# Kernel optimization log

Measured on AMD Instinct MI355X. Metric: run time of the kernel, lower is better.

## Reference

```python
import jax, jax.numpy as jnp
import numpy as np

BN_EPS = 1e-5


def setup_inputs() -> dict:
    key = jax.random.key(0)
    ks = jax.random.split(key, 8)
    B, S, D = 2048, 64, 128      # batch, seq_len, d_in
    H, DK = 8, 16                # n_head, d_k; H*DK == 128
    F = H * DK
    std = np.sqrt(2.0 / DK).astype(np.float32)
    return {
        "v": jax.random.normal(ks[0], (B, S, D), jnp.float32),
        "Wq": jax.random.normal(ks[1], (F, D), jnp.float32) * std,
        "bq": jnp.zeros((F,), jnp.float32),
        "bn_gamma": jnp.ones((F,), jnp.float32),
        "bn_beta": jnp.zeros((F,), jnp.float32),
        "W2": jax.random.normal(ks[2], (F, F), jnp.float32) * (1.0 / np.sqrt(F)),
        "b2": jnp.zeros((F,), jnp.float32),
        "Wk": jax.random.normal(ks[3], (F, D), jnp.float32) * std,
        "bk": jnp.zeros((F,), jnp.float32),
    }


def reference(v, Wq, bq, bn_gamma, bn_beta, W2, b2, Wk, bk):
    # v: [B, S, D]
    B, S, D = v.shape
    F = Wq.shape[0]
    H = 8
    DK = F // H
    temperature = jnp.asarray(np.sqrt(DK), v.dtype)

    # q path: linear -> mean over seq -> BatchNorm1d (batch stats) -> linear
    q = jnp.einsum("bsd,fd->bsf", v, Wq) + bq          # [B, S, F]
    q = q.mean(axis=1)                                  # [B, F]
    mu = q.mean(axis=0)
    var = q.var(axis=0)                                 # biased, as BN uses
    q = (q - mu) * jax.lax.rsqrt(var + BN_EPS) * bn_gamma + bn_beta
    q = jnp.einsum("bf,gf->bg", q, W2) + b2             # [B, F]
    q = q.reshape(B, H, DK).transpose(1, 0, 2)          # [H, B, DK]

    # k path
    k = (jnp.einsum("bsd,fd->bsf", v, Wk) + bk).reshape(B, S, H, DK)
    k = k.transpose(2, 0, 1, 3)                         # [H, B, S, DK]

    # single query per (head, batch): scores over seq
    attn = jnp.einsum("hbd,hbsd->hbs", q, k) / temperature
    attn = jax.nn.softmax(attn, axis=-1)                # [H, B, S]
    # dropout is identity in eval mode

    # weighted sum over seq of the ORIGINAL v (torch repeats v per head;
    # broadcasting avoids materializing the repeat)
    out = jnp.einsum("hbs,bsd->hbd", attn, v)           # [H, B, D]
    return out, attn
```

## Files before the change

kernel.cpp:

```cpp
#include <hip/hip_runtime.h>

#define B_ 2048
#define S_ 64
#define D_ 128
#define F_ 128
#define H_ 8

__global__ __launch_bounds__(256) void k_q1(const float* __restrict__ v,
                                            const float* __restrict__ Wq,
                                            const float* __restrict__ bq,
                                            float* __restrict__ q1) {
  const int b = blockIdx.x;
  const int t = threadIdx.x;
  __shared__ float red[8 * 128];
  __shared__ __align__(16) float vbarL[128];

  const int c4 = t & 31;
  const int r0 = t >> 5;
  const float4* v4 = (const float4*)(v + (size_t)b * (S_ * D_));
  float4 acc = {0.f, 0.f, 0.f, 0.f};
  #pragma unroll
  for (int i = 0; i < 8; ++i) {
    float4 x = v4[(r0 * 8 + i) * 32 + c4];
    acc.x += x.x; acc.y += x.y; acc.z += x.z; acc.w += x.w;
  }
  red[r0 * 128 + c4 * 4 + 0] = acc.x;
  red[r0 * 128 + c4 * 4 + 1] = acc.y;
  red[r0 * 128 + c4 * 4 + 2] = acc.z;
  red[r0 * 128 + c4 * 4 + 3] = acc.w;
  __syncthreads();
  if (t < 128) {
    float s = 0.f;
    #pragma unroll
    for (int r = 0; r < 8; ++r) s += red[r * 128 + t];
    vbarL[t] = s * (1.0f / 64.0f);
  }
  __syncthreads();

  const float4* Wq4 = (const float4*)Wq;
  const float4* vb4 = (const float4*)vbarL;
  const int d4 = t & 31;
  const int fg = t >> 5;
  #pragma unroll
  for (int fi = 0; fi < 16; ++fi) {
    int f = fi * 8 + fg;
    float4 w = Wq4[f * 32 + d4];
    float4 vv = vb4[d4];
    float p = w.x * vv.x + w.y * vv.y + w.z * vv.z + w.w * vv.w;
    #pragma unroll
    for (int off = 16; off; off >>= 1) p += __shfl_down(p, off, 32);
    if (d4 == 0) q1[b * F_ + f] = p + bq[f];
  }
}

__global__ __launch_bounds__(256) void k_stats(const float* __restrict__ q1,
                                               const float* __restrict__ gamma,
                                               const float* __restrict__ beta,
                                               float* __restrict__ sscale,
                                               float* __restrict__ sshift) {
  const int f = blockIdx.x;
  const int t = threadIdx.x;
  float s = 0.f, sq = 0.f;
  #pragma unroll
  for (int i = 0; i < 8; ++i) {
    float x = q1[(i * 256 + t) * F_ + f];
    s += x;
    sq += x * x;
  }
  #pragma unroll
  for (int off = 32; off; off >>= 1) {
    s += __shfl_down(s, off, 64);
    sq += __shfl_down(sq, off, 64);
  }
  __shared__ float rs_[4], rq_[4];
  const int w = t >> 6;
  if ((t & 63) == 0) { rs_[w] = s; rq_[w] = sq; }
  __syncthreads();
  if (t == 0) {
    s = rs_[0] + rs_[1] + rs_[2] + rs_[3];
    sq = rq_[0] + rq_[1] + rq_[2] + rq_[3];
    float mu = s * (1.0f / (float)B_);
    float var = sq * (1.0f / (float)B_) - mu * mu;
    float rsg = rsqrtf(var + 1e-5f) * gamma[f];
    sscale[f] = rsg;
    sshift[f] = beta[f] - mu * rsg;
  }
}

__global__ __launch_bounds__(256) void k_qw(const float* __restrict__ q1,
                                            const float* __restrict__ sscale,
                                            const float* __restrict__ sshift,
                                            const float* __restrict__ W2,
                                            const float* __restrict__ b2,
                                            const float* __restrict__ Wk,
                                            const float* __restrict__ bk,
                                            float* __restrict__ qW,
                                            float* __restrict__ qb) {
  const int b0 = blockIdx.x * 8;
  const int t = threadIdx.x;
  __shared__ __align__(16) float W2L[128 * 128];
  __shared__ __align__(16) float qnL[8 * 128];
  __shared__ __align__(16) float q2L[8 * 128];

  float4* W2L4 = (float4*)W2L;
  const float4* W2g4 = (const float4*)W2;
  #pragma unroll
  for (int i = 0; i < 16; ++i) {
    int idx4 = i * 256 + t;
    int g = idx4 >> 5, f4 = idx4 & 31;
    W2L4[g * 32 + (f4 ^ (g & 31))] = W2g4[idx4];
  }
  #pragma unroll
  for (int i = 0; i < 4; ++i) {
    int idx = i * 256 + t;
    int bi = idx >> 7, f = idx & 127;
    qnL[idx] = q1[(b0 + bi) * F_ + f] * sscale[f] + sshift[f];
  }
  __syncthreads();

  const float4* qnL4 = (const float4*)qnL;
  #pragma unroll
  for (int i = 0; i < 4; ++i) {
    int o = i * 256 + t;
    int bi = o >> 7, g = o & 127;
    float acc = b2[g];
    #pragma unroll
    for (int f4 = 0; f4 < 32; ++f4) {
      float4 qv = qnL4[bi * 32 + f4];
      float4 wv = W2L4[g * 32 + (f4 ^ (g & 31))];
      acc += qv.x * wv.x + qv.y * wv.y + qv.z * wv.z + qv.w * wv.w;
    }
    q2L[bi * 128 + g] = acc;
  }
  __syncthreads();

  const float4* Wk4 = (const float4*)Wk;
  #pragma unroll
  for (int i = 0; i < 8; ++i) {
    int o4 = i * 256 + t;
    int bi = o4 >> 8, h = (o4 >> 5) & 7, d4 = o4 & 31;
    float4 acc = {0.f, 0.f, 0.f, 0.f};
    const float* q2row = &q2L[bi * 128 + h * 16];
    #pragma unroll
    for (int dk = 0; dk < 16; ++dk) {
      float q = q2row[dk];
      float4 w = Wk4[(h * 16 + dk) * 32 + d4];
      acc.x += q * w.x; acc.y += q * w.y; acc.z += q * w.z; acc.w += q * w.w;
    }
    ((float4*)qW)[(size_t)(b0 + bi) * 256 + h * 32 + d4] = acc;
  }
  if (t < 64) {
    int bi = t >> 3, h = t & 7;
    float acc = 0.f;
    #pragma unroll
    for (int dk = 0; dk < 16; ++dk)
      acc += q2L[bi * 128 + h * 16 + dk] * bk[h * 16 + dk];
    qb[(b0 + bi) * 8 + h] = acc;
  }
}

__global__ __launch_bounds__(256) void k_attn(const float* __restrict__ v,
                                              const float* __restrict__ qW,
                                              const float* __restrict__ qb,
                                              float* __restrict__ outp) {
  const int b = blockIdx.x;
  const int t = threadIdx.x;
  __shared__ __align__(16) float vL[64 * 128];
  __shared__ __align__(16) float qWL[8 * 128];
  __shared__ float attnL[8 * 64];
  __shared__ float qbL[8];

  float4* vL4 = (float4*)vL;
  const float4* vg4 = (const float4*)(v + (size_t)b * (S_ * D_));
  #pragma unroll
  for (int i = 0; i < 8; ++i) {
    int idx = i * 256 + t;
    int s = idx >> 5, c4 = idx & 31;
    vL4[s * 32 + (c4 ^ (s & 31))] = vg4[idx];
  }
  {
    const float4* qWg4 = (const float4*)(qW + (size_t)b * (H_ * D_));
    ((float4*)qWL)[t] = qWg4[t];
  }
  if (t < 8) qbL[t] = qb[b * 8 + t];
  __syncthreads();

  const int s = t & 63;
  const int hq = t >> 6;
  const int h0 = hq * 2, h1 = hq * 2 + 1;
  const float4* qWL4 = (const float4*)qWL;
  float a0 = 0.f, a1 = 0.f;
  #pragma unroll
  for (int d4 = 0; d4 < 32; ++d4) {
    float4 vv = vL4[s * 32 + (d4 ^ (s & 31))];
    float4 w0 = qWL4[h0 * 32 + d4];
    float4 w1 = qWL4[h1 * 32 + d4];
    a0 += vv.x * w0.x + vv.y * w0.y + vv.z * w0.z + vv.w * w0.w;
    a1 += vv.x * w1.x + vv.y * w1.y + vv.z * w1.z + vv.w * w1.w;
  }
  float l0 = (a0 + qbL[h0]) * 0.25f;
  float l1 = (a1 + qbL[h1]) * 0.25f;

  float m0 = l0, m1 = l1;
  #pragma unroll
  for (int off = 32; off; off >>= 1) {
    m0 = fmaxf(m0, __shfl_xor(m0, off, 64));
    m1 = fmaxf(m1, __shfl_xor(m1, off, 64));
  }
  float e0 = __expf(l0 - m0), e1 = __expf(l1 - m1);
  float s0 = e0, s1 = e1;
  #pragma unroll
  for (int off = 32; off; off >>= 1) {
    s0 += __shfl_xor(s0, off, 64);
    s1 += __shfl_xor(s1, off, 64);
  }
  float at0 = e0 / s0, at1 = e1 / s1;
  attnL[h0 * 64 + s] = at0;
  attnL[h1 * 64 + s] = at1;
  float* attn_out = outp + (size_t)H_ * B_ * D_;
  attn_out[(size_t)h0 * (B_ * S_) + b * S_ + s] = at0;
  attn_out[(size_t)h1 * (B_ * S_) + b * S_ + s] = at1;
  __syncthreads();

  const int d4o = t & 31;
  const int h = t >> 5;
  float4 acc = {0.f, 0.f, 0.f, 0.f};
  #pragma unroll
  for (int si = 0; si < 64; ++si) {
    float a = attnL[h * 64 + si];
    float4 vv = vL4[si * 32 + (d4o ^ (si & 31))];
    acc.x += a * vv.x; acc.y += a * vv.y; acc.z += a * vv.z; acc.w += a * vv.w;
  }
  ((float4*)outp)[(size_t)h * (B_ * 32) + b * 32 + d4o] = acc;
}

extern "C" void kernel_launch(void* const* d_in, const int* in_sizes, int n_in,
                              void* d_out, int out_size, void* d_ws, size_t ws_size,
                              hipStream_t stream) {
  const float* v     = (const float*)d_in[0];
  const float* Wq    = (const float*)d_in[1];
  const float* bq    = (const float*)d_in[2];
  const float* gamma = (const float*)d_in[3];
  const float* beta  = (const float*)d_in[4];
  const float* W2    = (const float*)d_in[5];
  const float* b2    = (const float*)d_in[6];
  const float* Wk    = (const float*)d_in[7];
  const float* bk    = (const float*)d_in[8];

  float* ws = (float*)d_ws;
  float* q1v    = ws;
  float* sscale = ws + (size_t)B_ * F_;
  float* sshift = sscale + 128;
  float* qWv    = sshift + 128;
  float* qbv    = qWv + (size_t)B_ * H_ * D_;
  float* outp   = (float*)d_out;

  hipLaunchKernelGGL(k_q1,    dim3(B_),  dim3(256), 0, stream, v, Wq, bq, q1v);
  hipLaunchKernelGGL(k_stats, dim3(F_),  dim3(256), 0, stream, q1v, gamma, beta, sscale, sshift);
  hipLaunchKernelGGL(k_qw,    dim3(256), dim3(256), 0, stream, q1v, sscale, sshift, W2, b2, Wk, bk, qWv, qbv);
  hipLaunchKernelGGL(k_attn,  dim3(B_),  dim3(256), 0, stream, v, qWv, qbv, outp);
}
```

Baseline: 69.42 us.

## Restructure BN stats and q2 path; fold Wk projection into attention kernel

Replaces the per-feature stats kernel (128 blocks doing strided column reads) with 64 blocks that read rows coalesced and combine partial sums through global atomics after a memset. The same kernel also transposes W2. The q2 kernel then reads W2t straight from global memory instead of staging a swizzled 64KB copy in LDS per block, and writes only q2. The qW = q2·Wk projection and the bias term move into k_attn, so the qW intermediate is no longer written and re-read from global memory. In exchange this adds a memset launch and atomics whose summation order is nondeterministic.

```diff
diff --git a/kernel.cpp b/kernel.cpp
--- a/kernel.cpp
+++ b/kernel.cpp
@@ -53,120 +53,98 @@
   }
 }
 
-__global__ __launch_bounds__(256) void k_stats(const float* __restrict__ q1,
-                                               const float* __restrict__ gamma,
-                                               const float* __restrict__ beta,
-                                               float* __restrict__ sscale,
-                                               float* __restrict__ sshift) {
-  const int f = blockIdx.x;
-  const int t = threadIdx.x;
-  float s = 0.f, sq = 0.f;
-  #pragma unroll
-  for (int i = 0; i < 8; ++i) {
-    float x = q1[(i * 256 + t) * F_ + f];
-    s += x;
-    sq += x * x;
-  }
-  #pragma unroll
-  for (int off = 32; off; off >>= 1) {
-    s += __shfl_down(s, off, 64);
-    sq += __shfl_down(sq, off, 64);
-  }
-  __shared__ float rs_[4], rq_[4];
-  const int w = t >> 6;
-  if ((t & 63) == 0) { rs_[w] = s; rq_[w] = sq; }
-  __syncthreads();
-  if (t == 0) {
-    s = rs_[0] + rs_[1] + rs_[2] + rs_[3];
-    sq = rq_[0] + rq_[1] + rq_[2] + rq_[3];
-    float mu = s * (1.0f / (float)B_);
-    float var = sq * (1.0f / (float)B_) - mu * mu;
-    float rsg = rsqrtf(var + 1e-5f) * gamma[f];
-    sscale[f] = rsg;
-    sshift[f] = beta[f] - mu * rsg;
-  }
-}
-
-__global__ __launch_bounds__(256) void k_qw(const float* __restrict__ q1,
-                                            const float* __restrict__ sscale,
-                                            const float* __restrict__ sshift,
-                                            const float* __restrict__ W2,
+__global__ __launch_bounds__(256) void k_stats2(const float* __restrict__ q1,
+                                                const float* __restrict__ W2,
+                                                float* __restrict__ gsum,
+                                                float* __restrict__ gsq,
+                                                float* __restrict__ W2t) {
+  const int blk = blockIdx.x;
+  const int t = threadIdx.x;
+  const int f4 = t & 31, rg = t >> 5;
+  const int r0 = blk * 32;
+  const float4* q14 = (const float4*)q1;
+  float4 s = {0.f, 0.f, 0.f, 0.f};
+  float4 q = {0.f, 0.f, 0.f, 0.f};
+  #pragma unroll
+  for (int k = 0; k < 4; ++k) {
+    float4 x = q14[(size_t)(r0 + rg + 8 * k) * 32 + f4];
+    s.x += x.x; s.y += x.y; s.z += x.z; s.w += x.w;
+    q.x += x.x * x.x; q.y += x.y * x.y; q.z += x.z * x.z; q.w += x.w * x.w;
+  }
+  __shared__ float rs[8][128], rq[8][128];
+  rs[rg][f4 * 4 + 0] = s.x; rs[rg][f4 * 4 + 1] = s.y;
+  rs[rg][f4 * 4 + 2] = s.z; rs[rg][f4 * 4 + 3] = s.w;
+  rq[rg][f4 * 4 + 0] = q.x; rq[rg][f4 * 4 + 1] = q.y;
+  rq[rg][f4 * 4 + 2] = q.z; rq[rg][f4 * 4 + 3] = q.w;
+  __syncthreads();
+  if (t < 128) {
+    float ss = 0.f, qq = 0.f;
+    #pragma unroll
+    for (int r = 0; r < 8; ++r) { ss += rs[r][t]; qq += rq[r][t]; }
+    atomicAdd(&gsum[t], ss);
+    atomicAdd(&gsq[t], qq);
+  }
+  {
+    int g = blk * 2 + (t >> 7);
+    int f = t & 127;
+    W2t[f * 128 + g] = W2[g * 128 + f];
+  }
+}
+
+__global__ __launch_bounds__(256) void k_q2(const float* __restrict__ q1,
+                                            const float* __restrict__ gsum,
+                                            const float* __restrict__ gsq,
+                                            const float* __restrict__ gamma,
+                                            const float* __restrict__ beta,
+                                            const float* __restrict__ W2t,
                                             const float* __restrict__ b2,
-                                            const float* __restrict__ Wk,
-                                            const float* __restrict__ bk,
-                                            float* __restrict__ qW,
-                                            float* __restrict__ qb) {
+                                            float* __restrict__ q2) {
   const int b0 = blockIdx.x * 8;
   const int t = threadIdx.x;
-  __shared__ __align__(16) float W2L[128 * 128];
+  __shared__ float scaleL[128], shiftL[128];
   __shared__ __align__(16) float qnL[8 * 128];
-  __shared__ __align__(16) float q2L[8 * 128];
-
-  float4* W2L4 = (float4*)W2L;
-  const float4* W2g4 = (const float4*)W2;
-  #pragma unroll
-  for (int i = 0; i < 16; ++i) {
-    int idx4 = i * 256 + t;
-    int g = idx4 >> 5, f4 = idx4 & 31;
-    W2L4[g * 32 + (f4 ^ (g & 31))] = W2g4[idx4];
-  }
-  #pragma unroll
-  for (int i = 0; i < 4; ++i) {
-    int idx = i * 256 + t;
-    int bi = idx >> 7, f = idx & 127;
-    qnL[idx] = q1[(b0 + bi) * F_ + f] * sscale[f] + sshift[f];
-  }
-  __syncthreads();
-
-  const float4* qnL4 = (const float4*)qnL;
-  #pragma unroll
-  for (int i = 0; i < 4; ++i) {
-    int o = i * 256 + t;
-    int bi = o >> 7, g = o & 127;
-    float acc = b2[g];
-    #pragma unroll
-    for (int f4 = 0; f4 < 32; ++f4) {
-      float4 qv = qnL4[bi * 32 + f4];
-      float4 wv = W2L4[g * 32 + (f4 ^ (g & 31))];
-      acc += qv.x * wv.x + qv.y * wv.y + qv.z * wv.z + qv.w * wv.w;
-    }
-    q2L[bi * 128 + g] = acc;
-  }
-  __syncthreads();
-
-  const float4* Wk4 = (const float4*)Wk;
-  #pragma unroll
-  for (int i = 0; i < 8; ++i) {
-    int o4 = i * 256 + t;
-    int bi = o4 >> 8, h = (o4 >> 5) & 7, d4 = o4 & 31;
-    float4 acc = {0.f, 0.f, 0.f, 0.f};
-    const float* q2row = &q2L[bi * 128 + h * 16];
-    #pragma unroll
-    for (int dk = 0; dk < 16; ++dk) {
-      float q = q2row[dk];
-      float4 w = Wk4[(h * 16 + dk) * 32 + d4];
-      acc.x += q * w.x; acc.y += q * w.y; acc.z += q * w.z; acc.w += q * w.w;
-    }
-    ((float4*)qW)[(size_t)(b0 + bi) * 256 + h * 32 + d4] = acc;
-  }
-  if (t < 64) {
-    int bi = t >> 3, h = t & 7;
-    float acc = 0.f;
-    #pragma unroll
-    for (int dk = 0; dk < 16; ++dk)
-      acc += q2L[bi * 128 + h * 16 + dk] * bk[h * 16 + dk];
-    qb[(b0 + bi) * 8 + h] = acc;
-  }
+
+  if (t < 128) {
+    float mu = gsum[t] * (1.0f / (float)B_);
+    float var = gsq[t] * (1.0f / (float)B_) - mu * mu;
+    float rsg = rsqrtf(var + 1e-5f) * gamma[t];
+    scaleL[t] = rsg;
+    shiftL[t] = beta[t] - mu * rsg;
+  }
+  __syncthreads();
+  {
+    int row = t >> 5, f4 = t & 31;
+    float4 x = ((const float4*)q1)[(size_t)(b0 + row) * 32 + f4];
+    x.x = x.x * scaleL[f4 * 4 + 0] + shiftL[f4 * 4 + 0];
+    x.y = x.y * scaleL[f4 * 4 + 1] + shiftL[f4 * 4 + 1];
+    x.z = x.z * scaleL[f4 * 4 + 2] + shiftL[f4 * 4 + 2];
+    x.w = x.w * scaleL[f4 * 4 + 3] + shiftL[f4 * 4 + 3];
+    ((float4*)qnL)[row * 32 + f4] = x;
+  }
+  __syncthreads();
+
+  const int r = t >> 5, g4 = t & 31;
+  const float4* W2t4 = (const float4*)W2t;
+  float4 acc = ((const float4*)b2)[g4];
+  #pragma unroll 8
+  for (int f = 0; f < 128; ++f) {
+    float4 w = W2t4[f * 32 + g4];
+    float qv = qnL[r * 128 + f];
+    acc.x += qv * w.x; acc.y += qv * w.y; acc.z += qv * w.z; acc.w += qv * w.w;
+  }
+  ((float4*)q2)[(size_t)(b0 + r) * 32 + g4] = acc;
 }
 
 __global__ __launch_bounds__(256) void k_attn(const float* __restrict__ v,
-                                              const float* __restrict__ qW,
-                                              const float* __restrict__ qb,
+                                              const float* __restrict__ q2,
+                                              const float* __restrict__ Wk,
+                                              const float* __restrict__ bk,
                                               float* __restrict__ outp) {
   const int b = blockIdx.x;
   const int t = threadIdx.x;
   __shared__ __align__(16) float vL[64 * 128];
   __shared__ __align__(16) float qWL[8 * 128];
+  __shared__ __align__(16) float q2L[128];
   __shared__ float attnL[8 * 64];
   __shared__ float qbL[8];
 
@@ -178,11 +156,29 @@
     int s = idx >> 5, c4 = idx & 31;
     vL4[s * 32 + (c4 ^ (s & 31))] = vg4[idx];
   }
+  if (t < 32) ((float4*)q2L)[t] = ((const float4*)q2)[(size_t)b * 32 + t];
+  __syncthreads();
+
   {
-    const float4* qWg4 = (const float4*)(qW + (size_t)b * (H_ * D_));
-    ((float4*)qWL)[t] = qWg4[t];
-  }
-  if (t < 8) qbL[t] = qb[b * 8 + t];
+    const int h = t >> 5, d4 = t & 31;
+    const float4* Wk4 = (const float4*)Wk;
+    const float* q2row = &q2L[h * 16];
+    float4 acc = {0.f, 0.f, 0.f, 0.f};
+    #pragma unroll
+    for (int dk = 0; dk < 16; ++dk) {
+      float qv = q2row[dk];
+      float4 w = Wk4[(h * 16 + dk) * 32 + d4];
+      acc.x += qv * w.x; acc.y += qv * w.y; acc.z += qv * w.z; acc.w += qv * w.w;
+    }
+    ((float4*)qWL)[h * 32 + d4] = acc;
+  }
+  if (t < 8) {
+    float acc = 0.f;
+    #pragma unroll
+    for (int dk = 0; dk < 16; ++dk)
+      acc += q2L[t * 16 + dk] * bk[t * 16 + dk];
+    qbL[t] = acc;
+  }
   __syncthreads();
 
   const int s = t & 63;
@@ -248,15 +244,16 @@
   const float* bk    = (const float*)d_in[8];
 
   float* ws = (float*)d_ws;
-  float* q1v    = ws;
-  float* sscale = ws + (size_t)B_ * F_;
-  float* sshift = sscale + 128;
-  float* qWv    = sshift + 128;
-  float* qbv    = qWv + (size_t)B_ * H_ * D_;
-  float* outp   = (float*)d_out;
-
-  hipLaunchKernelGGL(k_q1,    dim3(B_),  dim3(256), 0, stream, v, Wq, bq, q1v);
-  hipLaunchKernelGGL(k_stats, dim3(F_),  dim3(256), 0, stream, q1v, gamma, beta, sscale, sshift);
-  hipLaunchKernelGGL(k_qw,    dim3(256), dim3(256), 0, stream, q1v, sscale, sshift, W2, b2, Wk, bk, qWv, qbv);
-  hipLaunchKernelGGL(k_attn,  dim3(B_),  dim3(256), 0, stream, v, qWv, qbv, outp);
-}
+  float* q1v  = ws;
+  float* q2v  = q1v + (size_t)B_ * F_;
+  float* gsum = q2v + (size_t)B_ * F_;
+  float* gsq  = gsum + 128;
+  float* W2t  = gsq + 128;
+  float* outp = (float*)d_out;
+
+  hipMemsetAsync(gsum, 0, 2 * 128 * sizeof(float), stream);
+  hipLaunchKernelGGL(k_q1,     dim3(B_),  dim3(256), 0, stream, v, Wq, bq, q1v);
+  hipLaunchKernelGGL(k_stats2, dim3(64),  dim3(256), 0, stream, q1v, W2, gsum, gsq, W2t);
+  hipLaunchKernelGGL(k_q2,     dim3(256), dim3(256), 0, stream, q1v, gsum, gsq, gamma, beta, W2t, b2, q2v);
+  hipLaunchKernelGGL(k_attn,   dim3(B_),  dim3(256), 0, stream, v, q2v, Wk, bk, outp);
+}
```

Result: faster. 65.23 us (-6.0%).
